# Kernel tuning notes

Hardware: AMD Instinct MI355X
Metric: run time of the kernel (lower is better)

## Reference

```python
import jax, jax.numpy as jnp
import numpy as np

N = 8          # num_tasks (PHQ-8)
D_EMB = 64     # task_embed_dim
HID = 128      # hidden_dim
L = 2          # num_gat_layers
H = 4          # num_heads
B = 16384      # batch size

CLUSTERS = {'core_depression': [0, 1, 5], 'cognitive': [6, 7], 'somatic': [2, 3, 4]}
CROSS = [(0, 6), (0, 7), (1, 6), (1, 7), (5, 6), (5, 7), (0, 2), (0, 3), (1, 2), (1, 3), (1, 4), (6, 2), (7, 3)]


def build_graph():
    adj = np.eye(N, dtype=np.int32)
    et = np.zeros((N, N), dtype=np.int32)
    for idxs in CLUSTERS.values():
        for i in idxs:
            for j in idxs:
                adj[i, j] = 1
                if i != j:
                    et[i, j] = 1
    for i, j in CROSS:
        adj[i, j] = 1
        adj[j, i] = 1
        et[i, j] = 2
        et[j, i] = 2
    return adj, et


def setup_inputs() -> dict:
    key = jax.random.key(0)
    ks = jax.random.split(key, 10)
    adj, et = build_graph()
    s = 0.05
    return {
        'shared_embedding': jax.random.normal(ks[0], (B, HID), dtype=jnp.float32),
        'task_embeddings': jax.random.normal(ks[1], (N, D_EMB), dtype=jnp.float32) * s,
        'W_in': jax.random.normal(ks[2], (HID, D_EMB), dtype=jnp.float32) * s,
        'b_in': jnp.zeros((HID,), dtype=jnp.float32),
        'W_heads': jax.random.normal(ks[3], (L, H, HID, HID), dtype=jnp.float32) * s,
        'a_heads': jax.random.normal(ks[4], (L, H, 2 * HID), dtype=jnp.float32) * s,
        'out_W': jax.random.normal(ks[5], (L, HID, H * HID), dtype=jnp.float32) * s,
        'out_b': jnp.zeros((L, HID), dtype=jnp.float32),
        'ln_scale': jnp.ones((L, HID), dtype=jnp.float32),
        'ln_bias': jnp.zeros((L, HID), dtype=jnp.float32),
        'omega_intra': jnp.asarray(1.0, dtype=jnp.float32),
        'omega_cross': jnp.asarray(0.6, dtype=jnp.float32),
        'adj': jnp.asarray(adj),
        'edge_types': jnp.asarray(et),
    }


def reference(shared_embedding, task_embeddings, W_in, b_in, W_heads, a_heads,
              out_W, out_b, ln_scale, ln_bias, omega_intra, omega_cross, adj, edge_types):
    adjf = adj.astype(jnp.float32)
    # learnable edge weights: intra-cluster omega_intra, cross-cluster omega_cross, zero off-edge
    ew = jnp.ones_like(adjf)
    ew = jnp.where(edge_types == 1, omega_intra, ew)
    ew = jnp.where(edge_types == 2, omega_cross, ew)
    ew = ew * adjf  # [N, N]

    b = shared_embedding.shape[0]
    h_task = task_embeddings @ W_in.T + b_in          # [N, HID]
    h = h_task[None, :, :] + shared_embedding[:, None, :]  # [B, N, HID]

    n_layers = W_heads.shape[0]
    for l in range(n_layers):
        # per-head projection: Linear(y = x W^T), W_heads[l]: [H, out, in]
        Wh = jnp.einsum('bnf,hgf->bhng', h, W_heads[l])  # [B, H, N, F]
        f = Wh.shape[-1]
        a_src = a_heads[l][:, :f]   # [H, F]
        a_dst = a_heads[l][:, f:]   # [H, F]
        # concat-based additive score decomposed into two dot products
        ei = jnp.einsum('bhnf,hf->bhn', Wh, a_src)
        ej = jnp.einsum('bhnf,hf->bhn', Wh, a_dst)
        e = jax.nn.leaky_relu(ei[:, :, :, None] + ej[:, :, None, :], 0.2)  # [B,H,N,N]
        att = jnp.where(adjf[None, None] > 0, e, jnp.float32(-9e15))
        # faithful to original: masked entries multiplied by (zero) edge weights -> 0 logits
        att = att * ew[None, None]
        att = jax.nn.softmax(att, axis=-1)
        hp = jax.nn.elu(jnp.einsum('bhnm,bhmf->bhnf', att, Wh))  # [B,H,N,F]
        hcat = jnp.moveaxis(hp, 1, 2).reshape(b, hp.shape[2], -1)  # [B,N,H*F]
        gout = hcat @ out_W[l].T + out_b[l]  # [B,N,HID]
        # residual + layernorm
        x = h + gout
        mu = x.mean(-1, keepdims=True)
        var = x.var(-1, keepdims=True)
        h = (x - mu) / jnp.sqrt(var + 1e-5) * ln_scale[l] + ln_bias[l]
    return h, ew
```

## Files before the change

### kernel.cpp

```cpp
#include <hip/hip_runtime.h>
#include <stdint.h>

typedef __attribute__((ext_vector_type(8))) short bf16x8;
typedef __attribute__((ext_vector_type(4))) float f32x4;
typedef unsigned long long ull;

typedef uint4 uint4_a __attribute__((may_alias));
typedef ull ull_a __attribute__((may_alias));
typedef bf16x8 bf16x8_a __attribute__((may_alias));

#define LGKM0() __builtin_amdgcn_s_waitcnt(0xc07f)
#define MFMA16(a, b, c) __builtin_amdgcn_mfma_f32_16x16x32_bf16((a), (b), (c), 0, 0, 0)

__device__ __forceinline__ unsigned f2bf(float x) {
    unsigned u = __float_as_uint(x);
    return (u + 0x7fffu + ((u >> 16) & 1u)) >> 16;
}
__device__ __forceinline__ float bf2f(short s) {
    return __uint_as_float(((unsigned)(unsigned short)s) << 16);
}
__device__ __forceinline__ ull pack4(f32x4 v) {
    return (ull)f2bf(v.x) | ((ull)f2bf(v.y) << 16) | ((ull)f2bf(v.z) << 32) | ((ull)f2bf(v.w) << 48);
}

__global__ void gat_prep(const float* __restrict__ te, const float* __restrict__ W_in,
                         const float* __restrict__ b_in, const float* __restrict__ W_heads,
                         const float* __restrict__ a_heads, const float* __restrict__ om_i,
                         const float* __restrict__ om_c, const int* __restrict__ adj,
                         const int* __restrict__ et, const float* __restrict__ out_W,
                         unsigned short* __restrict__ wsW1, unsigned short* __restrict__ wsW2,
                         unsigned short* __restrict__ wsWsd, float* __restrict__ wsHt,
                         float* __restrict__ wsEw, float* __restrict__ eout) {
    const int gid = blockIdx.x, tid = threadIdx.x;
    if (gid < 1024) {
        int idx = gid * 256 + tid;
        if (idx < 131072) wsW1[idx] = (unsigned short)f2bf(W_heads[idx]);
        else wsW2[idx - 131072] = (unsigned short)f2bf(out_W[idx - 131072]);
    } else if (gid < 1028) {
        int idx = (gid - 1024) * 256 + tid;
        int n = idx >> 7, o = idx & 127;
        float s = b_in[o];
        for (int f = 0; f < 64; ++f) s += te[n * 64 + f] * W_in[o * 64 + f];
        wsHt[idx] = s;
    } else if (gid < 1044) {
        int idx = (gid - 1028) * 256 + tid;
        int l = idx >> 11, p = (idx >> 7) & 15, f = idx & 127;
        float s = 0.f;
        if (p < 8) {
            int hh = p >> 1, ss = p & 1;
            const float* a = a_heads + (l * 4 + hh) * 256 + ss * 128;
            const float* Wb = W_heads + (l * 4 + hh) * 16384;
            for (int g = 0; g < 128; ++g) s += a[g] * Wb[g * 128 + f];
        }
        wsWsd[idx] = (unsigned short)f2bf(s);
    } else {
        if (tid < 64) {
            float v = 0.f;
            if (adj[tid]) {
                int t = et[tid];
                v = (t == 1) ? om_i[0] : ((t == 2) ? om_c[0] : 1.0f);
            }
            wsEw[tid] = v;
            eout[tid] = v;
        }
    }
}

__device__ __forceinline__ void load_chunk(int chunk, int tid,
                                           const unsigned short* __restrict__ wsW1,
                                           const unsigned short* __restrict__ wsW2, uint4* pf) {
    const int l = chunk >> 3, h = (chunk >> 1) & 3;
    const int r = tid >> 2, part = tid & 3;
    const unsigned short* src = (chunk & 1) ? (wsW2 + ((l << 7) + r) * 512 + (h << 7) + part * 32)
                                            : (wsW1 + (((l << 2) + h) * 128 + r) * 128 + part * 32);
#pragma unroll
    for (int k = 0; k < 4; ++k) pf[k] = *(const uint4_a*)(src + 8 * k);
}

__global__ __launch_bounds__(512, 1) void gat_main(
    const float* __restrict__ shared_emb, const float* __restrict__ out_b,
    const float* __restrict__ ln_s, const float* __restrict__ ln_b,
    const unsigned short* __restrict__ wsW1, const unsigned short* __restrict__ wsW2,
    const unsigned short* __restrict__ wsWsd, const float* __restrict__ wsHt,
    const float* __restrict__ wsEw, float* __restrict__ out) {
    __shared__ __align__(16) unsigned short sW[128 * 136];
    __shared__ __align__(16) unsigned short sScr[8][5120];
    __shared__ __align__(16) float sE[8][32][8];
    __shared__ __align__(16) unsigned short sAtt[8][32][8];

    const int tid = threadIdx.x;
    const int w = tid >> 6, lane = tid & 63, q = lane >> 4, c = lane & 15;
    const long wrow0 = (long)blockIdx.x * 256 + (long)w * 32;

    float ewr[8];
#pragma unroll
    for (int m = 0; m < 8; ++m) ewr[m] = wsEw[(lane & 7) * 8 + m];

    bf16x8 xf[2][4];
#pragma unroll
    for (int mt = 0; mt < 2; ++mt) {
        const long row = wrow0 + 16 * mt + c;
        const size_t b = (size_t)(row >> 3);
        const int t = (int)(row & 7);
#pragma unroll
        for (int kk = 0; kk < 4; ++kk) {
            const int f0 = 32 * kk + 8 * q;
            const float4 s0 = *(const float4*)(shared_emb + b * 128 + f0);
            const float4 s1 = *(const float4*)(shared_emb + b * 128 + f0 + 4);
            const float4 h0 = *(const float4*)(wsHt + t * 128 + f0);
            const float4 h1 = *(const float4*)(wsHt + t * 128 + f0 + 4);
            float v[8] = {s0.x + h0.x, s0.y + h0.y, s0.z + h0.z, s0.w + h0.w,
                          s1.x + h1.x, s1.y + h1.y, s1.z + h1.z, s1.w + h1.w};
            bf16x8 r;
#pragma unroll
            for (int j = 0; j < 8; ++j) r[j] = (short)f2bf(v[j]);
            xf[mt][kk] = r;
        }
    }

    f32x4 gacc[8][2];
    uint4 pf[4];
    load_chunk(0, tid, wsW1, wsW2, pf);

    for (int chunk = 0; chunk < 16; ++chunk) {
        const int l = chunk >> 3, h = (chunk >> 1) & 3, isW2 = chunk & 1;
        {
            const int r = tid >> 2, part = tid & 3;
            unsigned short* dst = &sW[r * 136 + part * 32];
#pragma unroll
            for (int k = 0; k < 4; ++k) *(uint4_a*)(dst + 8 * k) = pf[k];
        }
        if (chunk < 15) load_chunk(chunk + 1, tid, wsW1, wsW2, pf);
        __syncthreads();

        if (!isW2) {
            if (h == 0) {
                const f32x4 z4 = {0.f, 0.f, 0.f, 0.f};
#pragma unroll
                for (int ot = 0; ot < 8; ++ot)
#pragma unroll
                    for (int nt = 0; nt < 2; ++nt) gacc[ot][nt] = z4;
                f32x4 e[2] = {z4, z4};
#pragma unroll
                for (int kk = 0; kk < 4; ++kk) {
                    bf16x8 bw = *(const bf16x8_a*)(wsWsd + ((l << 4) + c) * 128 + 32 * kk + 8 * q);
#pragma unroll
                    for (int mt = 0; mt < 2; ++mt) e[mt] = MFMA16(xf[mt][kk], bw, e[mt]);
                }
                if (c < 8) {
#pragma unroll
                    for (int mt = 0; mt < 2; ++mt)
#pragma unroll
                        for (int r = 0; r < 4; ++r) sE[w][16 * mt + 4 * q + r][c] = e[mt][r];
                }
                LGKM0();
            }
            if (lane < 32) {
                const int r = lane, eb = r & 24;
                const float ei = sE[w][r][2 * h];
                float lgt[8];
#pragma unroll
                for (int m = 0; m < 8; ++m) {
                    float s = ei + sE[w][eb + m][2 * h + 1];
                    s = s > 0.f ? s : 0.2f * s;
                    lgt[m] = s * ewr[m];
                }
                float mx = lgt[0];
#pragma unroll
                for (int m = 1; m < 8; ++m) mx = fmaxf(mx, lgt[m]);
                float p[8], sum = 0.f;
#pragma unroll
                for (int m = 0; m < 8; ++m) {
                    p[m] = __expf(lgt[m] - mx);
                    sum += p[m];
                }
                const float inv = 1.0f / sum;
                uint4 av;
                av.x = f2bf(p[0] * inv) | (f2bf(p[1] * inv) << 16);
                av.y = f2bf(p[2] * inv) | (f2bf(p[3] * inv) << 16);
                av.z = f2bf(p[4] * inv) | (f2bf(p[5] * inv) << 16);
                av.w = f2bf(p[6] * inv) | (f2bf(p[7] * inv) << 16);
                *(uint4_a*)&sAtt[w][r][0] = av;
            }
            f32x4 acc[16];
            {
                const f32x4 z4 = {0.f, 0.f, 0.f, 0.f};
#pragma unroll
                for (int i = 0; i < 16; ++i) acc[i] = z4;
            }
#pragma unroll
            for (int kk = 0; kk < 4; ++kk)
#pragma unroll
                for (int gt = 0; gt < 8; ++gt) {
                    bf16x8 bw = *(const bf16x8_a*)&sW[(16 * gt + c) * 136 + 32 * kk + 8 * q];
#pragma unroll
                    for (int mt = 0; mt < 2; ++mt)
                        acc[mt * 8 + gt] = MFMA16(xf[mt][kk], bw, acc[mt * 8 + gt]);
                }
            LGKM0();
#pragma unroll
            for (int gt = 0; gt < 8; ++gt)
#pragma unroll
                for (int mt = 0; mt < 2; ++mt)
                    *(ull_a*)&sScr[w][(16 * gt + c) * 40 + 16 * mt + 4 * q] = pack4(acc[mt * 8 + gt]);
            LGKM0();
            bf16x8 bat[2];
#pragma unroll
            for (int nt = 0; nt < 2; ++nt) {
                const int n = 16 * nt + c;
                bf16x8 zb;
#pragma unroll
                for (int j = 0; j < 8; ++j) zb[j] = 0;
                bat[nt] = (q == 2 * nt + (c >> 3)) ? *(const bf16x8_a*)&sAtt[w][n][0] : zb;
            }
            {
                const f32x4 z4 = {0.f, 0.f, 0.f, 0.f};
#pragma unroll
                for (int i = 0; i < 16; ++i) acc[i] = z4;
            }
#pragma unroll
            for (int ct = 0; ct < 8; ++ct) {
                bf16x8 a0 = *(const bf16x8_a*)&sScr[w][(16 * ct + c) * 40 + 8 * q];
#pragma unroll
                for (int nt = 0; nt < 2; ++nt)
                    acc[ct * 2 + nt] = MFMA16(a0, bat[nt], acc[ct * 2 + nt]);
            }
            LGKM0();
#pragma unroll
            for (int ct = 0; ct < 8; ++ct)
#pragma unroll
                for (int nt = 0; nt < 2; ++nt) {
                    f32x4 v = acc[ct * 2 + nt];
#pragma unroll
                    for (int j = 0; j < 4; ++j) {
                        float x = v[j];
                        v[j] = x > 0.f ? x : (__expf(x) - 1.f);
                    }
                    *(ull_a*)&sScr[w][(16 * nt + c) * 136 + 16 * ct + 4 * q] = pack4(v);
                }
            LGKM0();
        } else {
#pragma unroll
            for (int kk = 0; kk < 4; ++kk) {
                bf16x8 bh[2];
#pragma unroll
                for (int nt = 0; nt < 2; ++nt)
                    bh[nt] = *(const bf16x8_a*)&sScr[w][(16 * nt + c) * 136 + 32 * kk + 8 * q];
#pragma unroll
                for (int ot = 0; ot < 8; ++ot) {
                    bf16x8 aw = *(const bf16x8_a*)&sW[(16 * ot + c) * 136 + 32 * kk + 8 * q];
#pragma unroll
                    for (int nt = 0; nt < 2; ++nt) gacc[ot][nt] = MFMA16(aw, bh[nt], gacc[ot][nt]);
                }
            }
            if (h == 3) {
                LGKM0();
#pragma unroll
                for (int ot = 0; ot < 8; ++ot)
#pragma unroll
                    for (int nt = 0; nt < 2; ++nt)
                        *(ull_a*)&sScr[w][(16 * nt + c) * 136 + 16 * ot + 4 * q] = pack4(gacc[ot][nt]);
                LGKM0();
                const float* ob = out_b + l * 128;
                float sum[2] = {0.f, 0.f}, ssq[2] = {0.f, 0.f};
#pragma unroll
                for (int mt = 0; mt < 2; ++mt)
#pragma unroll
                    for (int kk = 0; kk < 4; ++kk) {
                        bf16x8 g8 = *(const bf16x8_a*)&sScr[w][(16 * mt + c) * 136 + 32 * kk + 8 * q];
                        bf16x8 x8 = xf[mt][kk];
                        const int f0 = 32 * kk + 8 * q;
#pragma unroll
                        for (int j = 0; j < 8; ++j) {
                            float x = bf2f(g8[j]) + bf2f(x8[j]) + ob[f0 + j];
                            sum[mt] += x;
                            ssq[mt] += x * x;
                        }
                    }
                float mu[2], rs[2];
#pragma unroll
                for (int mt = 0; mt < 2; ++mt) {
                    sum[mt] += __shfl_xor(sum[mt], 16);
                    sum[mt] += __shfl_xor(sum[mt], 32);
                    ssq[mt] += __shfl_xor(ssq[mt], 16);
                    ssq[mt] += __shfl_xor(ssq[mt], 32);
                    mu[mt] = sum[mt] * (1.0f / 128.0f);
                    float var = ssq[mt] * (1.0f / 128.0f) - mu[mt] * mu[mt];
                    rs[mt] = rsqrtf(var + 1e-5f);
                }
                const float* lsc = ln_s + l * 128;
                const float* lbi = ln_b + l * 128;
#pragma unroll
                for (int mt = 0; mt < 2; ++mt) {
                    const long row = wrow0 + 16 * mt + c;
#pragma unroll
                    for (int kk = 0; kk < 4; ++kk) {
                        bf16x8 g8 = *(const bf16x8_a*)&sScr[w][(16 * mt + c) * 136 + 32 * kk + 8 * q];
                        bf16x8 x8 = xf[mt][kk];
                        const int f0 = 32 * kk + 8 * q;
                        float y[8];
#pragma unroll
                        for (int j = 0; j < 8; ++j) {
                            float x = bf2f(g8[j]) + bf2f(x8[j]) + ob[f0 + j];
                            y[j] = (x - mu[mt]) * rs[mt] * lsc[f0 + j] + lbi[f0 + j];
                        }
                        if (l == 0) {
                            bf16x8 r;
#pragma unroll
                            for (int j = 0; j < 8; ++j) r[j] = (short)f2bf(y[j]);
                            xf[mt][kk] = r;
                        } else {
                            float4 o0 = {y[0], y[1], y[2], y[3]};
                            float4 o1 = {y[4], y[5], y[6], y[7]};
                            *(float4*)(out + (size_t)row * 128 + f0) = o0;
                            *(float4*)(out + (size_t)row * 128 + f0 + 4) = o1;
                        }
                    }
                }
            }
        }
        __syncthreads();
    }
}

extern "C" void kernel_launch(void* const* d_in, const int* in_sizes, int n_in, void* d_out,
                              int out_size, void* d_ws, size_t ws_size, hipStream_t stream) {
    const float* shared_emb = (const float*)d_in[0];
    const float* te = (const float*)d_in[1];
    const float* W_in = (const float*)d_in[2];
    const float* b_in = (const float*)d_in[3];
    const float* W_heads = (const float*)d_in[4];
    const float* a_heads = (const float*)d_in[5];
    const float* out_W = (const float*)d_in[6];
    const float* out_b = (const float*)d_in[7];
    const float* ln_s = (const float*)d_in[8];
    const float* ln_b = (const float*)d_in[9];
    const float* om_i = (const float*)d_in[10];
    const float* om_c = (const float*)d_in[11];
    const int* adj = (const int*)d_in[12];
    const int* et = (const int*)d_in[13];
    float* out = (float*)d_out;

    unsigned short* wsW1 = (unsigned short*)d_ws;
    unsigned short* wsW2 = wsW1 + 131072;
    unsigned short* wsWsd = wsW2 + 131072;
    float* wsHt = (float*)((char*)d_ws + 532480);
    float* wsEw = wsHt + 1024;

    float* eout = out + (out_size - 64);

    gat_prep<<<1045, 256, 0, stream>>>(te, W_in, b_in, W_heads, a_heads, om_i, om_c, adj, et,
                                       out_W, wsW1, wsW2, wsWsd, wsHt, wsEw, eout);

    const int B = in_sizes[0] / 128;
    const int grid = (B * 8) / 256;
    gat_main<<<grid, 512, 0, stream>>>(shared_emb, out_b, ln_s, ln_b, wsW1, wsW2, wsWsd, wsHt,
                                       wsEw, out);
}
```

Before: 353.4 us.

## Pre-swizzle weights into MFMA fragment order and read directly from global

The prep kernel now writes the bf16 weights pre-arranged in MFMA fragment layout, so the main kernel loads B/A operands straight from global/L2 instead of staging each chunk through shared memory. This removes the per-chunk shared-memory weight copy and the block-wide __syncthreads, letting waves run independently. Blocks shrink to 256 threads with two blocks per CU. The layernorm epilogue keeps the GAT output in fp32 in shared memory and coalesces the final output stores. The trade-off is that every wave re-reads the full weight set from cache rather than sharing one LDS copy.

Measured after the change: 369.2 us. 1.04x slower.

```diff
diff --git a/kernel.cpp b/kernel.cpp
--- a/kernel.cpp
+++ b/kernel.cpp
@@ -8,6 +8,7 @@
 typedef uint4 uint4_a __attribute__((may_alias));
 typedef ull ull_a __attribute__((may_alias));
 typedef bf16x8 bf16x8_a __attribute__((may_alias));
+typedef f32x4 f32x4_a __attribute__((may_alias));
 
 #define LGKM0() __builtin_amdgcn_s_waitcnt(0xc07f)
 #define MFMA16(a, b, c) __builtin_amdgcn_mfma_f32_16x16x32_bf16((a), (b), (c), 0, 0, 0)
@@ -28,18 +29,26 @@
                          const float* __restrict__ a_heads, const float* __restrict__ om_i,
                          const float* __restrict__ om_c, const int* __restrict__ adj,
                          const int* __restrict__ et, const float* __restrict__ out_W,
-                         unsigned short* __restrict__ wsW1, unsigned short* __restrict__ wsW2,
-                         unsigned short* __restrict__ wsWsd, float* __restrict__ wsHt,
-                         float* __restrict__ wsEw, float* __restrict__ eout) {
+                         unsigned short* __restrict__ wsWf, unsigned short* __restrict__ wsWsd,
+                         float* __restrict__ wsHt, float* __restrict__ wsEw,
+                         float* __restrict__ eout) {
     const int gid = blockIdx.x, tid = threadIdx.x;
     if (gid < 1024) {
         int idx = gid * 256 + tid;
-        if (idx < 131072) wsW1[idx] = (unsigned short)f2bf(W_heads[idx]);
-        else wsW2[idx - 131072] = (unsigned short)f2bf(out_W[idx - 131072]);
+        int j = idx & 7, lane = (idx >> 3) & 63, frag = (idx >> 9) & 31, chunk = idx >> 14;
+        int cc = lane & 15, qq = lane >> 4, kk = frag >> 3, t = frag & 7;
+        int l = chunk >> 3, h = (chunk >> 1) & 3;
+        float v;
+        if (chunk & 1)
+            v = out_W[(l * 128 + 16 * t + cc) * 512 + 128 * h + 32 * kk + 8 * qq + j];
+        else
+            v = W_heads[((l * 4 + h) * 128 + 16 * t + cc) * 128 + 32 * kk + 8 * qq + j];
+        wsWf[idx] = (unsigned short)f2bf(v);
     } else if (gid < 1028) {
         int idx = (gid - 1024) * 256 + tid;
         int n = idx >> 7, o = idx & 127;
         float s = b_in[o];
+#pragma unroll 8
         for (int f = 0; f < 64; ++f) s += te[n * 64 + f] * W_in[o * 64 + f];
         wsHt[idx] = s;
     } else if (gid < 1044) {
@@ -50,6 +59,7 @@
             int hh = p >> 1, ss = p & 1;
             const float* a = a_heads + (l * 4 + hh) * 256 + ss * 128;
             const float* Wb = W_heads + (l * 4 + hh) * 16384;
+#pragma unroll 8
             for (int g = 0; g < 128; ++g) s += a[g] * Wb[g * 128 + f];
         }
         wsWsd[idx] = (unsigned short)f2bf(s);
@@ -66,35 +76,18 @@
     }
 }
 
-__device__ __forceinline__ void load_chunk(int chunk, int tid,
-                                           const unsigned short* __restrict__ wsW1,
-                                           const unsigned short* __restrict__ wsW2, uint4* pf) {
-    const int l = chunk >> 3, h = (chunk >> 1) & 3;
-    const int r = tid >> 2, part = tid & 3;
-    const unsigned short* src = (chunk & 1) ? (wsW2 + ((l << 7) + r) * 512 + (h << 7) + part * 32)
-                                            : (wsW1 + (((l << 2) + h) * 128 + r) * 128 + part * 32);
-#pragma unroll
-    for (int k = 0; k < 4; ++k) pf[k] = *(const uint4_a*)(src + 8 * k);
-}
-
-__global__ __launch_bounds__(512, 1) void gat_main(
+__global__ __launch_bounds__(256, 2) void gat_main(
     const float* __restrict__ shared_emb, const float* __restrict__ out_b,
     const float* __restrict__ ln_s, const float* __restrict__ ln_b,
-    const unsigned short* __restrict__ wsW1, const unsigned short* __restrict__ wsW2,
-    const unsigned short* __restrict__ wsWsd, const float* __restrict__ wsHt,
-    const float* __restrict__ wsEw, float* __restrict__ out) {
-    __shared__ __align__(16) unsigned short sW[128 * 136];
-    __shared__ __align__(16) unsigned short sScr[8][5120];
-    __shared__ __align__(16) float sE[8][32][8];
-    __shared__ __align__(16) unsigned short sAtt[8][32][8];
+    const unsigned short* __restrict__ wsWf, const unsigned short* __restrict__ wsWsd,
+    const float* __restrict__ wsHt, const float* __restrict__ wsEw, float* __restrict__ out) {
+    __shared__ __align__(16) unsigned short sScr[4][5120];
+    __shared__ __align__(16) float sE[4][32][8];
+    __shared__ __align__(16) unsigned short sAtt[4][32][8];
 
     const int tid = threadIdx.x;
     const int w = tid >> 6, lane = tid & 63, q = lane >> 4, c = lane & 15;
-    const long wrow0 = (long)blockIdx.x * 256 + (long)w * 32;
-
-    float ewr[8];
-#pragma unroll
-    for (int m = 0; m < 8; ++m) ewr[m] = wsEw[(lane & 7) * 8 + m];
+    const long wrow0 = (long)blockIdx.x * 128 + (long)w * 32;
 
     bf16x8 xf[2][4];
 #pragma unroll
@@ -119,20 +112,10 @@
     }
 
     f32x4 gacc[8][2];
-    uint4 pf[4];
-    load_chunk(0, tid, wsW1, wsW2, pf);
 
     for (int chunk = 0; chunk < 16; ++chunk) {
         const int l = chunk >> 3, h = (chunk >> 1) & 3, isW2 = chunk & 1;
-        {
-            const int r = tid >> 2, part = tid & 3;
-            unsigned short* dst = &sW[r * 136 + part * 32];
-#pragma unroll
-            for (int k = 0; k < 4; ++k) *(uint4_a*)(dst + 8 * k) = pf[k];
-        }
-        if (chunk < 15) load_chunk(chunk + 1, tid, wsW1, wsW2, pf);
-        __syncthreads();
-
+        const unsigned short* __restrict__ wf = wsWf + (size_t)chunk * 16384 + (size_t)lane * 8;
         if (!isW2) {
             if (h == 0) {
                 const f32x4 z4 = {0.f, 0.f, 0.f, 0.f};
@@ -163,7 +146,7 @@
                 for (int m = 0; m < 8; ++m) {
                     float s = ei + sE[w][eb + m][2 * h + 1];
                     s = s > 0.f ? s : 0.2f * s;
-                    lgt[m] = s * ewr[m];
+                    lgt[m] = s * wsEw[(r & 7) * 8 + m];
                 }
                 float mx = lgt[0];
 #pragma unroll
@@ -182,6 +165,8 @@
                 av.w = f2bf(p[6] * inv) | (f2bf(p[7] * inv) << 16);
                 *(uint4_a*)&sAtt[w][r][0] = av;
             }
+            LGKM0();
+
             f32x4 acc[16];
             {
                 const f32x4 z4 = {0.f, 0.f, 0.f, 0.f};
@@ -192,17 +177,17 @@
             for (int kk = 0; kk < 4; ++kk)
 #pragma unroll
                 for (int gt = 0; gt < 8; ++gt) {
-                    bf16x8 bw = *(const bf16x8_a*)&sW[(16 * gt + c) * 136 + 32 * kk + 8 * q];
+                    bf16x8 bw = *(const bf16x8_a*)(wf + (size_t)(kk * 8 + gt) * 512);
 #pragma unroll
                     for (int mt = 0; mt < 2; ++mt)
                         acc[mt * 8 + gt] = MFMA16(xf[mt][kk], bw, acc[mt * 8 + gt]);
                 }
-            LGKM0();
 #pragma unroll
             for (int gt = 0; gt < 8; ++gt)
 #pragma unroll
                 for (int mt = 0; mt < 2; ++mt)
-                    *(ull_a*)&sScr[w][(16 * gt + c) * 40 + 16 * mt + 4 * q] = pack4(acc[mt * 8 + gt]);
+                    *(ull_a*)&sScr[w][(16 * gt + c) * 40 + 16 * mt + 4 * q] =
+                        pack4(acc[mt * 8 + gt]);
             LGKM0();
             bf16x8 bat[2];
 #pragma unroll
@@ -248,78 +233,87 @@
                     bh[nt] = *(const bf16x8_a*)&sScr[w][(16 * nt + c) * 136 + 32 * kk + 8 * q];
 #pragma unroll
                 for (int ot = 0; ot < 8; ++ot) {
-                    bf16x8 aw = *(const bf16x8_a*)&sW[(16 * ot + c) * 136 + 32 * kk + 8 * q];
+                    bf16x8 aw = *(const bf16x8_a*)(wf + (size_t)(kk * 8 + ot) * 512);
 #pragma unroll
                     for (int nt = 0; nt < 2; ++nt) gacc[ot][nt] = MFMA16(aw, bh[nt], gacc[ot][nt]);
                 }
             }
             if (h == 3) {
                 LGKM0();
-#pragma unroll
-                for (int ot = 0; ot < 8; ++ot)
-#pragma unroll
-                    for (int nt = 0; nt < 2; ++nt)
-                        *(ull_a*)&sScr[w][(16 * nt + c) * 136 + 16 * ot + 4 * q] = pack4(gacc[ot][nt]);
-                LGKM0();
+                float* sF = (float*)&sScr[w][0];
                 const float* ob = out_b + l * 128;
-                float sum[2] = {0.f, 0.f}, ssq[2] = {0.f, 0.f};
-#pragma unroll
-                for (int mt = 0; mt < 2; ++mt)
+                const float* lsc = ln_s + l * 128;
+                const float* lbi = ln_b + l * 128;
+#pragma unroll
+                for (int nt = 0; nt < 2; ++nt) {
+#pragma unroll
+                    for (int ot = 0; ot < 8; ++ot)
+                        *(f32x4_a*)&sF[c * 132 + 16 * ot + 4 * q] = gacc[ot][nt];
+                    LGKM0();
+                    float sum = 0.f, ssq = 0.f;
 #pragma unroll
                     for (int kk = 0; kk < 4; ++kk) {
-                        bf16x8 g8 = *(const bf16x8_a*)&sScr[w][(16 * mt + c) * 136 + 32 * kk + 8 * q];
-                        bf16x8 x8 = xf[mt][kk];
                         const int f0 = 32 * kk + 8 * q;
-#pragma unroll
-                        for (int j = 0; j < 8; ++j) {
-                            float x = bf2f(g8[j]) + bf2f(x8[j]) + ob[f0 + j];
-                            sum[mt] += x;
-                            ssq[mt] += x * x;
+                        f32x4 g0 = *(const f32x4_a*)&sF[c * 132 + f0];
+                        f32x4 g1 = *(const f32x4_a*)&sF[c * 132 + f0 + 4];
+                        bf16x8 x8 = xf[nt][kk];
+#pragma unroll
+                        for (int j = 0; j < 4; ++j) {
+                            float x = g0[j] + bf2f(x8[j]) + ob[f0 + j];
+                            sum += x;
+                            ssq += x * x;
+                            float x2 = g1[j] + bf2f(x8[4 + j]) + ob[f0 + 4 + j];
+                            sum += x2;
+                            ssq += x2 * x2;
                         }
                     }
-                float mu[2], rs[2];
-#pragma unroll
-                for (int mt = 0; mt < 2; ++mt) {
-                    sum[mt] += __shfl_xor(sum[mt], 16);
-                    sum[mt] += __shfl_xor(sum[mt], 32);
-                    ssq[mt] += __shfl_xor(ssq[mt], 16);
-                    ssq[mt] += __shfl_xor(ssq[mt], 32);
-                    mu[mt] = sum[mt] * (1.0f / 128.0f);
-                    float var = ssq[mt] * (1.0f / 128.0f) - mu[mt] * mu[mt];
-                    rs[mt] = rsqrtf(var + 1e-5f);
-                }
-                const float* lsc = ln_s + l * 128;
-                const float* lbi = ln_b + l * 128;
-#pragma unroll
-                for (int mt = 0; mt < 2; ++mt) {
-                    const long row = wrow0 + 16 * mt + c;
+                    sum += __shfl_xor(sum, 16);
+                    sum += __shfl_xor(sum, 32);
+                    ssq += __shfl_xor(ssq, 16);
+                    ssq += __shfl_xor(ssq, 32);
+                    const float mu = sum * (1.0f / 128.0f);
+                    const float var = ssq * (1.0f / 128.0f) - mu * mu;
+                    const float rs = rsqrtf(var + 1e-5f);
 #pragma unroll
                     for (int kk = 0; kk < 4; ++kk) {
-                        bf16x8 g8 = *(const bf16x8_a*)&sScr[w][(16 * mt + c) * 136 + 32 * kk + 8 * q];
-                        bf16x8 x8 = xf[mt][kk];
                         const int f0 = 32 * kk + 8 * q;
+                        f32x4 g0 = *(const f32x4_a*)&sF[c * 132 + f0];
+                        f32x4 g1 = *(const f32x4_a*)&sF[c * 132 + f0 + 4];
+                        bf16x8 x8 = xf[nt][kk];
                         float y[8];
 #pragma unroll
-                        for (int j = 0; j < 8; ++j) {
-                            float x = bf2f(g8[j]) + bf2f(x8[j]) + ob[f0 + j];
-                            y[j] = (x - mu[mt]) * rs[mt] * lsc[f0 + j] + lbi[f0 + j];
+                        for (int j = 0; j < 4; ++j) {
+                            float x = g0[j] + bf2f(x8[j]) + ob[f0 + j];
+                            y[j] = (x - mu) * rs * lsc[f0 + j] + lbi[f0 + j];
+                            float x2 = g1[j] + bf2f(x8[4 + j]) + ob[f0 + 4 + j];
+                            y[4 + j] = (x2 - mu) * rs * lsc[f0 + 4 + j] + lbi[f0 + 4 + j];
                         }
                         if (l == 0) {
                             bf16x8 r;
 #pragma unroll
                             for (int j = 0; j < 8; ++j) r[j] = (short)f2bf(y[j]);
-                            xf[mt][kk] = r;
+                            xf[nt][kk] = r;
                         } else {
-                            float4 o0 = {y[0], y[1], y[2], y[3]};
-                            float4 o1 = {y[4], y[5], y[6], y[7]};
-                            *(float4*)(out + (size_t)row * 128 + f0) = o0;
-                            *(float4*)(out + (size_t)row * 128 + f0 + 4) = o1;
+                            f32x4 o0 = {y[0], y[1], y[2], y[3]};
+                            f32x4 o1 = {y[4], y[5], y[6], y[7]};
+                            *(f32x4_a*)&sF[c * 132 + f0] = o0;
+                            *(f32x4_a*)&sF[c * 132 + f0 + 4] = o1;
                         }
                     }
+                    if (l == 1) {
+                        LGKM0();
+#pragma unroll
+                        for (int i = 0; i < 8; ++i) {
+                            const int flat = i * 256 + lane * 4;
+                            const int rr = flat >> 7, c0 = flat & 127;
+                            f32x4 v = *(const f32x4_a*)&sF[rr * 132 + c0];
+                            *(f32x4_a*)(out + (size_t)(wrow0 + 16 * nt + rr) * 128 + c0) = v;
+                        }
+                    }
+                    LGKM0();
                 }
             }
         }
-        __syncthreads();
     }
 }
 
@@ -341,19 +335,18 @@
     const int* et = (const int*)d_in[13];
     float* out = (float*)d_out;
 
-    unsigned short* wsW1 = (unsigned short*)d_ws;
-    unsigned short* wsW2 = wsW1 + 131072;
-    unsigned short* wsWsd = wsW2 + 131072;
+    unsigned short* wsWf = (unsigned short*)d_ws;
+    unsigned short* wsWsd = wsWf + 262144;
     float* wsHt = (float*)((char*)d_ws + 532480);
     float* wsEw = wsHt + 1024;
 
     float* eout = out + (out_size - 64);
 
     gat_prep<<<1045, 256, 0, stream>>>(te, W_in, b_in, W_heads, a_heads, om_i, om_c, adj, et,
-                                       out_W, wsW1, wsW2, wsWsd, wsHt, wsEw, eout);
+                                       out_W, wsWf, wsWsd, wsHt, wsEw, eout);
 
     const int B = in_sizes[0] / 128;
-    const int grid = (B * 8) / 256;
-    gat_main<<<grid, 512, 0, stream>>>(shared_emb, out_b, ln_s, ln_b, wsW1, wsW2, wsWsd, wsHt,
-                                       wsEw, out);
-}
+    const int grid = (B * 8) / 128;
+    gat_main<<<grid, 256, 0, stream>>>(shared_emb, out_b, ln_s, ln_b, wsWf, wsWsd, wsHt, wsEw,
+                                       out);
+}
```
